# Optimization experiments

Hardware: AMD Instinct MI355X
Metric: run time of the kernel (lower is better)

Reference implementation:

```python
import jax, jax.numpy as jnp
import numpy as np

NUM_HEADS = 12


def setup_inputs() -> dict:
    key = jax.random.key(0)
    ks = jax.random.split(key, 6)
    B, N, C = 16, 576, 768
    H, D = NUM_HEADS, 768 // NUM_HEADS
    P = 16
    x = jax.random.normal(ks[0], (B, N, C), dtype=jnp.float32)
    prompt = jax.random.normal(ks[1], (B, 2, P, H, D), dtype=jnp.float32)
    act_scale = jax.random.uniform(ks[2], (2,), dtype=jnp.float32)
    qkv_w = jax.random.normal(ks[3], (3 * C, C), dtype=jnp.float32) * (C ** -0.5)
    proj_w = jax.random.normal(ks[4], (C, C), dtype=jnp.float32) * (C ** -0.5)
    proj_b = jnp.zeros((C,), dtype=jnp.float32)
    return {"x": x, "prompt": prompt, "act_scale": act_scale,
            "qkv_w": qkv_w, "proj_w": proj_w, "proj_b": proj_b}


def reference(x, prompt, act_scale, qkv_w, proj_w, proj_b):
    B, N, C = x.shape
    H = NUM_HEADS
    D = C // H
    scale = D ** -0.5
    # qkv projection: [B,N,3C] -> (3,B,H,N,D)
    qkv = (x @ qkv_w.T).reshape(B, N, 3, H, D).transpose(2, 0, 3, 1, 4)
    q, k, v = qkv[0], qkv[1], qkv[2]
    # prompt: [B,2,P,H,D] -> (2,B,H,P,D)
    pr = jnp.transpose(prompt, (1, 0, 3, 2, 4))
    key_prefix, value_prefix = pr[0], pr[1]        # [B,H,P,D]
    v = jnp.concatenate([value_prefix, v], axis=2)  # [B,H,P+N,D]
    # gated prefix scores
    prompt_attn = jnp.einsum('bhnd,bhpd->bhnp', q, key_prefix) * scale
    prompt_attn = prompt_attn + jnp.tanh(prompt_attn * act_scale[0]) * act_scale[1]
    # standard scores
    attn = jnp.einsum('bhnd,bhmd->bhnm', q, k) * scale
    attn = jnp.concatenate([prompt_attn, attn], axis=-1)  # [B,H,N,P+N]
    attn = jax.nn.softmax(attn, axis=-1)
    out = jnp.einsum('bhnm,bhmd->bhnd', attn, v)  # [B,H,N,D]
    out = out.transpose(0, 2, 1, 3).reshape(B, N, C)
    return out @ proj_w.T + proj_b
```

## Files before the change

### kernel.cpp

```cpp
#include <hip/hip_runtime.h>
#include <hip/hip_bf16.h>
#include <math.h>

namespace {

constexpr int kB = 16, kN = 576, kC = 768, kH = 12, kP = 16;
constexpr int kM = kB * kN;

typedef __attribute__((ext_vector_type(8))) __bf16 bf16x8;
typedef __attribute__((ext_vector_type(4))) float  f32x4;
typedef __attribute__((ext_vector_type(8))) unsigned short u16x8;

__device__ inline unsigned short f2bf(float f) {
  __bf16 h = (__bf16)f;
  return __builtin_bit_cast(unsigned short, h);
}
__device__ inline float bf2f(unsigned short u) {
  unsigned int x = ((unsigned int)u) << 16;
  return __builtin_bit_cast(float, x);
}
__device__ inline unsigned int pk2bf(float lo, float hi) {
  return (unsigned int)f2bf(lo) | ((unsigned int)f2bf(hi) << 16);
}
__device__ inline int xcd_swz(int hw, int nwg) {
  const int per = nwg >> 3;
  return (hw & 7) * per + (hw >> 3);
}

__global__ __launch_bounds__(256)
void cvt3(const float* __restrict__ x, const float* __restrict__ wq,
          const float* __restrict__ wp, unsigned short* __restrict__ xo,
          unsigned short* __restrict__ wqo, unsigned short* __restrict__ wpo) {
  const int bid = blockIdx.x;
  const float* in; unsigned short* out; int base;
  if (bid < 6912)       { in = x;  out = xo;  base = bid; }
  else if (bid < 8640)  { in = wq; out = wqo; base = bid - 6912; }
  else                  { in = wp; out = wpo; base = bid - 8640; }
  const int i = base * 256 + threadIdx.x;
  const float4 v = ((const float4*)in)[i];
  ((ushort4*)out)[i] = make_ushort4(f2bf(v.x), f2bf(v.y), f2bf(v.z), f2bf(v.w));
}

template<int OB>
__global__ __launch_bounds__(256)
void gemm_bf16(const unsigned short* __restrict__ A, const unsigned short* __restrict__ W,
               const float* __restrict__ bias, void* __restrict__ Yv, int Kd, int Nd) {
  __shared__ __align__(16) unsigned short As[2][4096];
  __shared__ __align__(16) unsigned short Bs[2][4096];
  const int tid  = threadIdx.x;
  const int wv   = tid >> 6, lane = tid & 63;
  const int gx   = Nd >> 7;
  const int lg   = xcd_swz(blockIdx.x, gridDim.x);
  const long bm  = (long)(lg / gx) * 128;
  const long bn  = (long)(lg % gx) * 128;
  const int wr   = (wv >> 1) * 64;
  const int wc   = (wv & 1) * 64;
  const int row15 = lane & 15, kg = lane >> 4;

  auto stage = [&](int buf, int kt) {
#pragma unroll
    for (int site = 0; site < 2; ++site) {
      const int p = site * 256 + tid;
      const unsigned short* srcA = A + (bm + (p >> 2)) * (long)Kd + kt + (p & 3) * 8;
      const unsigned short* srcB = W + (bn + (p >> 2)) * (long)Kd + kt + (p & 3) * 8;
      __builtin_amdgcn_global_load_lds(
          (const __attribute__((address_space(1))) unsigned int*)srcA,
          (__attribute__((address_space(3))) unsigned int*)(&As[buf][site * 2048 + wv * 512]),
          16, 0, 0);
      __builtin_amdgcn_global_load_lds(
          (const __attribute__((address_space(1))) unsigned int*)srcB,
          (__attribute__((address_space(3))) unsigned int*)(&Bs[buf][site * 2048 + wv * 512]),
          16, 0, 0);
    }
  };

  f32x4 acc[4][4] = {};
  stage(0, 0);
  __syncthreads();

  const int nt = Kd >> 5;
  for (int t = 0; t < nt; ++t) {
    const int cur = t & 1;
    if (t + 1 < nt) stage(cur ^ 1, (t + 1) << 5);

    bf16x8 af[4], bf_[4];
#pragma unroll
    for (int mi = 0; mi < 4; ++mi)
      af[mi] = *(const bf16x8*)(&As[cur][(wr + mi * 16 + row15) * 32 + kg * 8]);
#pragma unroll
    for (int ni = 0; ni < 4; ++ni)
      bf_[ni] = *(const bf16x8*)(&Bs[cur][(wc + ni * 16 + row15) * 32 + kg * 8]);
#pragma unroll
    for (int mi = 0; mi < 4; ++mi)
#pragma unroll
      for (int ni = 0; ni < 4; ++ni)
        acc[mi][ni] = __builtin_amdgcn_mfma_f32_16x16x32_bf16(af[mi], bf_[ni], acc[mi][ni], 0, 0, 0);
    __syncthreads();
  }

  const int r4 = kg * 4;
#pragma unroll
  for (int ni = 0; ni < 4; ++ni) {
    const long col = bn + wc + ni * 16 + row15;
    if constexpr (OB) {
      unsigned short* Y = (unsigned short*)Yv;
#pragma unroll
      for (int mi = 0; mi < 4; ++mi)
#pragma unroll
        for (int j = 0; j < 4; ++j)
          Y[(bm + wr + mi * 16 + r4 + j) * (long)Nd + col] = f2bf(acc[mi][ni][j]);
    } else {
      float* Y = (float*)Yv;
      const float bv = bias ? bias[col] : 0.0f;
#pragma unroll
      for (int mi = 0; mi < 4; ++mi)
#pragma unroll
        for (int j = 0; j < 4; ++j)
          Y[(bm + wr + mi * 16 + r4 + j) * (long)Nd + col] = acc[mi][ni][j] + bv;
    }
  }
}

__global__ __launch_bounds__(384, 4)
void attn_mfma(const unsigned short* __restrict__ qkv, const float* __restrict__ prompt,
               const float* __restrict__ act_scale, unsigned short* __restrict__ attn_out) {
  const int lg = xcd_swz(blockIdx.x, gridDim.x);
  const int qt = lg % 6, bh = lg / 6;
  const int h = bh % kH, b = bh / kH;
  const int tid = threadIdx.x, wv = tid >> 6, lane = tid & 63;
  const int q15 = lane & 15, kg = lane >> 4;

  __shared__ __align__(16) unsigned short Klds[2][4096];
  __shared__ __align__(16) unsigned short Vt[2][4096];
  __shared__ __align__(16) unsigned short Plds[6][1024];

  const float a0 = act_scale[0], a1 = act_scale[1];
  const int sw  = q15 & 7;
  const int sl0 = (kg ^ sw) << 3;
  const int sl1 = ((4 + kg) ^ sw) << 3;

  bf16x8 qf[2];
  {
    const unsigned short* qrow = qkv + (size_t)(b * kN + qt * 96 + wv * 16 + q15) * 2304 + h * 64;
#pragma unroll
    for (int dh = 0; dh < 2; ++dh) {
      u16x8 raw = *(const u16x8*)(qrow + dh * 32 + kg * 8);
      u16x8 sc;
#pragma unroll
      for (int j = 0; j < 8; ++j) sc[j] = f2bf(bf2f(raw[j]) * 0.125f);
      qf[dh] = __builtin_bit_cast(bf16x8, sc);
    }
  }

  if (tid < 128) {
    const int r = tid >> 3, s = tid & 7;
    const float* src = prompt + (((size_t)(b * 2) * kP + r) * kH + h) * 64 + s * 8;
    const float4 f0 = *(const float4*)src, f1 = *(const float4*)(src + 4);
    *(uint4*)(&Klds[0][r * 64 + ((s ^ (r & 7)) << 3)]) =
        make_uint4(pk2bf(f0.x, f0.y), pk2bf(f0.z, f0.w), pk2bf(f1.x, f1.y), pk2bf(f1.z, f1.w));
  }
  if (tid < 256) {
    const int vkp = tid & 15, vdg = tid >> 4;
    unsigned int w[4] = {0, 0, 0, 0};
    if (vkp < 8) {
      const float* s0 = prompt + (((size_t)(b * 2 + 1) * kP + 2 * vkp) * kH + h) * 64 + vdg * 4;
      const float* s1 = s0 + kH * 64;
      const float4 x0 = *(const float4*)s0;
      const float4 y0 = *(const float4*)s1;
      w[0] = pk2bf(x0.x, y0.x); w[1] = pk2bf(x0.y, y0.y);
      w[2] = pk2bf(x0.z, y0.z); w[3] = pk2bf(x0.w, y0.w);
    }
#pragma unroll
    for (int j = 0; j < 4; ++j) {
      const int d = vdg * 4 + j;
      Plds[0][0] += 0;
      *(unsigned int*)(&Vt[0][d * 64 + (((vkp >> 2) ^ (d & 7)) << 3) + (vkp & 3) * 2]) = w[j];
    }
  }
  __syncthreads();

  f32x4 o[4] = {};
  float mrun = -3.0e38f, lrun = 0.0f;

  const int vkp = tid & 31;
  const int vdg = (tid >> 5) & 7;

  for (int ch = 0; ch < 10; ++ch) {
    const int cur = ch & 1;

    u16x8 vld0, vld1;
    const bool doV = (ch < 9) && (wv < 4);
    if (ch < 9) {
      if (doV) {
        const int nv = ch * 64 + 2 * vkp;
        const unsigned short* s0 = qkv + (size_t)(b * kN + nv) * 2304 + 1536 + h * 64 + vdg * 8;
        vld0 = *(const u16x8*)s0;
        vld1 = *(const u16x8*)(s0 + 2304);
      } else if (wv >= 4) {
        const int rbase = (wv - 4) * 32;
#pragma unroll
        for (int g = 0; g < 4; ++g) {
          const int r = rbase + g * 8 + (lane >> 3), s = lane & 7;
          const unsigned short* src =
              qkv + (size_t)(b * kN + ch * 64 + r) * 2304 + 768 + h * 64 + ((s ^ (r & 7)) << 3);
          __builtin_amdgcn_global_load_lds(
              (const __attribute__((address_space(1))) unsigned int*)src,
              (__attribute__((address_space(3))) unsigned int*)(&Klds[cur ^ 1][(rbase + g * 8) * 64]),
              16, 0, 0);
        }
      }
    }

    f32x4 c[4];
    const int nkb = (ch == 0) ? 1 : 4;
#pragma unroll
    for (int kb = 0; kb < 4; ++kb) {
      if (kb < nkb) {
        const unsigned short* krow = &Klds[cur][(kb * 16 + q15) * 64];
        const bf16x8 k0 = *(const bf16x8*)(krow + sl0);
        const bf16x8 k1 = *(const bf16x8*)(krow + sl1);
        f32x4 t = {};
        t = __builtin_amdgcn_mfma_f32_16x16x32_bf16(k0, qf[0], t, 0, 0, 0);
        c[kb] = __builtin_amdgcn_mfma_f32_16x16x32_bf16(k1, qf[1], t, 0, 0, 0);
      } else {
        c[kb][0] = c[kb][1] = c[kb][2] = c[kb][3] = -1.0e30f;
      }
    }
    if (ch == 0) {
#pragma unroll
      for (int j = 0; j < 4; ++j) {
        const float s = c[0][j];
        const float e = __expf(2.0f * s * a0);
        c[0][j] = s + ((e - 1.0f) / (e + 1.0f)) * a1;
      }
    }

    float cmax = -3.0e38f;
#pragma unroll
    for (int kb = 0; kb < 4; ++kb)
#pragma unroll
      for (int j = 0; j < 4; ++j) cmax = fmaxf(cmax, c[kb][j]);
    cmax = fmaxf(cmax, __shfl_xor(cmax, 16, 64));
    cmax = fmaxf(cmax, __shfl_xor(cmax, 32, 64));
    if (!__all(cmax - mrun <= 8.0f)) {
      const float mnew = fmaxf(mrun, cmax);
      const float resc = __expf(mrun - mnew);
      lrun *= resc;
      float rq[4];
#pragma unroll
      for (int jr = 0; jr < 4; ++jr) rq[jr] = __shfl(resc, kg * 4 + jr, 64);
#pragma unroll
      for (int nb = 0; nb < 4; ++nb)
#pragma unroll
        for (int jr = 0; jr < 4; ++jr) o[nb][jr] *= rq[jr];
      mrun = mnew;
    }
    float pe[16];
    float psum = 0.0f;
#pragma unroll
    for (int kb = 0; kb < 4; ++kb)
#pragma unroll
      for (int j = 0; j < 4; ++j) { pe[kb * 4 + j] = __expf(c[kb][j] - mrun); psum += pe[kb * 4 + j]; }
    psum += __shfl_xor(psum, 16, 64);
    psum += __shfl_xor(psum, 32, 64);
    lrun += psum;

    {
      unsigned short* pl = &Plds[wv][q15 * 64];
#pragma unroll
      for (int kb = 0; kb < 4; ++kb) {
        const int off = (((kb * 2 + (kg >> 1)) ^ sw) << 3) + (kg & 1) * 4;
        *(uint2*)(pl + off) = make_uint2(pk2bf(pe[kb * 4], pe[kb * 4 + 1]),
                                         pk2bf(pe[kb * 4 + 2], pe[kb * 4 + 3]));
      }
    }
    if (doV) {
#pragma unroll
      for (int j = 0; j < 8; ++j) {
        const int d = vdg * 8 + j;
        *(unsigned int*)(&Vt[cur ^ 1][d * 64 + (((vkp >> 2) ^ (d & 7)) << 3) + (vkp & 3) * 2]) =
            (unsigned int)vld0[j] | ((unsigned int)vld1[j] << 16);
      }
    }

    const unsigned short* pw = &Plds[wv][q15 * 64];
    const bf16x8 pa0 = *(const bf16x8*)(pw + sl0);
    const bf16x8 pa1 = *(const bf16x8*)(pw + sl1);
#pragma unroll
    for (int nb = 0; nb < 4; ++nb) {
      const unsigned short* vr = &Vt[cur][(nb * 16 + q15) * 64];
      const bf16x8 bv0 = *(const bf16x8*)(vr + sl0);
      o[nb] = __builtin_amdgcn_mfma_f32_16x16x32_bf16(pa0, bv0, o[nb], 0, 0, 0);
      if (ch != 0) {
        const bf16x8 bv1 = *(const bf16x8*)(vr + sl1);
        o[nb] = __builtin_amdgcn_mfma_f32_16x16x32_bf16(pa1, bv1, o[nb], 0, 0, 0);
      }
    }

    __syncthreads();
  }

  const float inv = 1.0f / lrun;
  float iq[4];
#pragma unroll
  for (int jr = 0; jr < 4; ++jr) iq[jr] = __shfl(inv, kg * 4 + jr, 64);
  unsigned short* obase = attn_out + (size_t)(b * kN + qt * 96 + wv * 16) * 768 + h * 64;
#pragma unroll
  for (int nb = 0; nb < 4; ++nb)
#pragma unroll
    for (int jr = 0; jr < 4; ++jr)
      obase[(size_t)(kg * 4 + jr) * 768 + nb * 16 + q15] = f2bf(o[nb][jr] * iq[jr]);
}

}

extern "C" void kernel_launch(void* const* d_in, const int* in_sizes, int n_in,
                              void* d_out, int out_size, void* d_ws, size_t ws_size,
                              hipStream_t stream) {
  const float* x         = (const float*)d_in[0];
  const float* prompt    = (const float*)d_in[1];
  const float* act_scale = (const float*)d_in[2];
  const float* qkv_w     = (const float*)d_in[3];
  const float* proj_w    = (const float*)d_in[4];
  const float* proj_b    = (const float*)d_in[5];
  float* out = (float*)d_out;

  char* ws = (char*)d_ws;
  unsigned short* qkvb   = (unsigned short*)ws;
  unsigned short* xa     = (unsigned short*)(ws + 42467328);
  unsigned short* qkvwb  = (unsigned short*)(ws + 42467328 + 14155776);
  unsigned short* projwb = (unsigned short*)(ws + 42467328 + 14155776 + 3538944);

  cvt3<<<9216, 256, 0, stream>>>(x, qkv_w, proj_w, xa, qkvwb, projwb);

  gemm_bf16<1><<<(3 * kC / 128) * (kM / 128), 256, 0, stream>>>(xa, qkvwb, nullptr, qkvb, kC, 3 * kC);
  attn_mfma<<<(kN / 96) * kH * kB, 384, 0, stream>>>(qkvb, prompt, act_scale, xa);
  gemm_bf16<0><<<(kC / 128) * (kM / 128), 256, 0, stream>>>(xa, projwb, proj_b, out, kC, kC);
}
```

Measured before the change: 136.4 us.

## Process two query tiles per wave in attention to reuse K/V fragments

The attention kernel drops from 6 waves of 16 query rows to 3 waves of 32 rows each, so every K and V fragment read from LDS feeds two MFMAs. V staging moves to 2 waves and K async loads to 1 wave. The prefix V padding is explicitly zeroed so the first chunk can run the full PV MFMA without a branch. s_setprio is added around the MFMA sections. The change trades fewer waves per block, and possibly lower occupancy, for more register reuse and fewer LDS reads.

After: 129.5 us. 5.1% less time.

```diff
diff --git a/kernel.cpp b/kernel.cpp
--- a/kernel.cpp
+++ b/kernel.cpp
@@ -26,6 +26,10 @@
   const int per = nwg >> 3;
   return (hw & 7) * per + (hw >> 3);
 }
+
+#define GLDS16(src, dst) __builtin_amdgcn_global_load_lds( \
+    (const __attribute__((address_space(1))) unsigned int*)(src), \
+    (__attribute__((address_space(3))) unsigned int*)(dst), 16, 0, 0)
 
 __global__ __launch_bounds__(256)
 void cvt3(const float* __restrict__ x, const float* __restrict__ wq,
@@ -63,14 +67,8 @@
       const int p = site * 256 + tid;
       const unsigned short* srcA = A + (bm + (p >> 2)) * (long)Kd + kt + (p & 3) * 8;
       const unsigned short* srcB = W + (bn + (p >> 2)) * (long)Kd + kt + (p & 3) * 8;
-      __builtin_amdgcn_global_load_lds(
-          (const __attribute__((address_space(1))) unsigned int*)srcA,
-          (__attribute__((address_space(3))) unsigned int*)(&As[buf][site * 2048 + wv * 512]),
-          16, 0, 0);
-      __builtin_amdgcn_global_load_lds(
-          (const __attribute__((address_space(1))) unsigned int*)srcB,
-          (__attribute__((address_space(3))) unsigned int*)(&Bs[buf][site * 2048 + wv * 512]),
-          16, 0, 0);
+      GLDS16(srcA, &As[buf][site * 2048 + wv * 512]);
+      GLDS16(srcB, &Bs[buf][site * 2048 + wv * 512]);
     }
   };
 
@@ -121,7 +119,46 @@
   }
 }
 
-__global__ __launch_bounds__(384, 4)
+__device__ inline void softmax_group(f32x4 (&c)[4], float& mrun, float& lrun,
+                                     f32x4 (&o)[4], unsigned short* pl,
+                                     const int kg, const int sw) {
+  float cmax = -3.0e38f;
+#pragma unroll
+  for (int kb = 0; kb < 4; ++kb)
+#pragma unroll
+    for (int j = 0; j < 4; ++j) cmax = fmaxf(cmax, c[kb][j]);
+  cmax = fmaxf(cmax, __shfl_xor(cmax, 16, 64));
+  cmax = fmaxf(cmax, __shfl_xor(cmax, 32, 64));
+  if (!__all(cmax - mrun <= 8.0f)) {
+    const float mnew = fmaxf(mrun, cmax);
+    const float resc = __expf(mrun - mnew);
+    lrun *= resc;
+    float rq[4];
+#pragma unroll
+    for (int jr = 0; jr < 4; ++jr) rq[jr] = __shfl(resc, kg * 4 + jr, 64);
+#pragma unroll
+    for (int nb = 0; nb < 4; ++nb)
+#pragma unroll
+      for (int jr = 0; jr < 4; ++jr) o[nb][jr] *= rq[jr];
+    mrun = mnew;
+  }
+  float psum = 0.0f;
+#pragma unroll
+  for (int kb = 0; kb < 4; ++kb) {
+    const float p0 = __expf(c[kb][0] - mrun);
+    const float p1 = __expf(c[kb][1] - mrun);
+    const float p2 = __expf(c[kb][2] - mrun);
+    const float p3 = __expf(c[kb][3] - mrun);
+    psum += (p0 + p1) + (p2 + p3);
+    const int off = (((kb * 2 + (kg >> 1)) ^ sw) << 3) + (kg & 1) * 4;
+    *(uint2*)(pl + off) = make_uint2(pk2bf(p0, p1), pk2bf(p2, p3));
+  }
+  psum += __shfl_xor(psum, 16, 64);
+  psum += __shfl_xor(psum, 32, 64);
+  lrun += psum;
+}
+
+__global__ __launch_bounds__(192, 3)
 void attn_mfma(const unsigned short* __restrict__ qkv, const float* __restrict__ prompt,
                const float* __restrict__ act_scale, unsigned short* __restrict__ attn_out) {
   const int lg = xcd_swz(blockIdx.x, gridDim.x);
@@ -132,184 +169,169 @@
 
   __shared__ __align__(16) unsigned short Klds[2][4096];
   __shared__ __align__(16) unsigned short Vt[2][4096];
-  __shared__ __align__(16) unsigned short Plds[6][1024];
+  __shared__ __align__(16) unsigned short Plds[3][2048];
 
   const float a0 = act_scale[0], a1 = act_scale[1];
   const int sw  = q15 & 7;
   const int sl0 = (kg ^ sw) << 3;
   const int sl1 = ((4 + kg) ^ sw) << 3;
 
-  bf16x8 qf[2];
-  {
-    const unsigned short* qrow = qkv + (size_t)(b * kN + qt * 96 + wv * 16 + q15) * 2304 + h * 64;
+  bf16x8 qf[2][2];
+#pragma unroll
+  for (int g = 0; g < 2; ++g) {
+    const unsigned short* qrow =
+        qkv + (size_t)(b * kN + qt * 96 + wv * 32 + g * 16 + q15) * 2304 + h * 64;
 #pragma unroll
     for (int dh = 0; dh < 2; ++dh) {
       u16x8 raw = *(const u16x8*)(qrow + dh * 32 + kg * 8);
       u16x8 sc;
 #pragma unroll
       for (int j = 0; j < 8; ++j) sc[j] = f2bf(bf2f(raw[j]) * 0.125f);
-      qf[dh] = __builtin_bit_cast(bf16x8, sc);
+      qf[g][dh] = __builtin_bit_cast(bf16x8, sc);
     }
   }
 
   if (tid < 128) {
     const int r = tid >> 3, s = tid & 7;
     const float* src = prompt + (((size_t)(b * 2) * kP + r) * kH + h) * 64 + s * 8;
-    const float4 f0 = *(const float4*)src, f1 = *(const float4*)(src + 4);
+    const f32x4 f0 = *(const f32x4*)src, f1 = *(const f32x4*)(src + 4);
     *(uint4*)(&Klds[0][r * 64 + ((s ^ (r & 7)) << 3)]) =
-        make_uint4(pk2bf(f0.x, f0.y), pk2bf(f0.z, f0.w), pk2bf(f1.x, f1.y), pk2bf(f1.z, f1.w));
-  }
-  if (tid < 256) {
-    const int vkp = tid & 15, vdg = tid >> 4;
-    unsigned int w[4] = {0, 0, 0, 0};
-    if (vkp < 8) {
-      const float* s0 = prompt + (((size_t)(b * 2 + 1) * kP + 2 * vkp) * kH + h) * 64 + vdg * 4;
-      const float* s1 = s0 + kH * 64;
-      const float4 x0 = *(const float4*)s0;
-      const float4 y0 = *(const float4*)s1;
-      w[0] = pk2bf(x0.x, y0.x); w[1] = pk2bf(x0.y, y0.y);
-      w[2] = pk2bf(x0.z, y0.z); w[3] = pk2bf(x0.w, y0.w);
-    }
+        make_uint4(pk2bf(f0[0], f0[1]), pk2bf(f0[2], f0[3]),
+                   pk2bf(f1[0], f1[1]), pk2bf(f1[2], f1[3]));
+  }
+  if (tid < 128) {
+    const int kp = tid & 7, vdq = tid >> 3;
+    const float* s0 = prompt + (((size_t)(b * 2 + 1) * kP + 2 * kp) * kH + h) * 64 + vdq * 4;
+    const f32x4 x0 = *(const f32x4*)s0;
+    const f32x4 y0 = *(const f32x4*)(s0 + kH * 64);
 #pragma unroll
     for (int j = 0; j < 4; ++j) {
-      const int d = vdg * 4 + j;
-      Plds[0][0] += 0;
-      *(unsigned int*)(&Vt[0][d * 64 + (((vkp >> 2) ^ (d & 7)) << 3) + (vkp & 3) * 2]) = w[j];
-    }
+      const int d = vdq * 4 + j;
+      *(unsigned int*)(&Vt[0][d * 64 + (((kp >> 2) ^ (d & 7)) << 3) + (kp & 3) * 2]) =
+          pk2bf(x0[j], y0[j]);
+    }
+  }
+#pragma unroll
+  for (int i = 0; i < 2; ++i) {
+    const int idx = tid + 192 * i;
+    const int d = idx / 6, szl = (idx % 6) + 2;
+    *(uint4*)(&Vt[0][d * 64 + ((szl ^ (d & 7)) << 3)]) = make_uint4(0, 0, 0, 0);
   }
   __syncthreads();
 
-  f32x4 o[4] = {};
-  float mrun = -3.0e38f, lrun = 0.0f;
-
-  const int vkp = tid & 31;
-  const int vdg = (tid >> 5) & 7;
+  f32x4 o0[4] = {}, o1[4] = {};
+  float m0 = -3.0e38f, l0 = 0.0f, m1 = -3.0e38f, l1 = 0.0f;
+
+  const int vkp  = tid & 31;
+  const int vdgb = tid >> 5;
+  const int kr8  = lane >> 3, ks8 = lane & 7;
 
   for (int ch = 0; ch < 10; ++ch) {
     const int cur = ch & 1;
 
-    u16x8 vld0, vld1;
-    const bool doV = (ch < 9) && (wv < 4);
+    u16x8 va0, va1, vb0, vb1;
+    const bool doV = (ch < 9) && (wv < 2);
     if (ch < 9) {
       if (doV) {
-        const int nv = ch * 64 + 2 * vkp;
-        const unsigned short* s0 = qkv + (size_t)(b * kN + nv) * 2304 + 1536 + h * 64 + vdg * 8;
-        vld0 = *(const u16x8*)s0;
-        vld1 = *(const u16x8*)(s0 + 2304);
-      } else if (wv >= 4) {
-        const int rbase = (wv - 4) * 32;
-#pragma unroll
-        for (int g = 0; g < 4; ++g) {
-          const int r = rbase + g * 8 + (lane >> 3), s = lane & 7;
+        const unsigned short* r0 = qkv + (size_t)(b * kN + ch * 64 + 2 * vkp) * 2304 + 1536 + h * 64;
+        va0 = *(const u16x8*)(r0 + vdgb * 8);
+        va1 = *(const u16x8*)(r0 + (vdgb + 4) * 8);
+        vb0 = *(const u16x8*)(r0 + 2304 + vdgb * 8);
+        vb1 = *(const u16x8*)(r0 + 2304 + (vdgb + 4) * 8);
+      } else if (wv == 2) {
+#pragma unroll
+        for (int g8 = 0; g8 < 8; ++g8) {
+          const int r = g8 * 8 + kr8;
           const unsigned short* src =
-              qkv + (size_t)(b * kN + ch * 64 + r) * 2304 + 768 + h * 64 + ((s ^ (r & 7)) << 3);
-          __builtin_amdgcn_global_load_lds(
-              (const __attribute__((address_space(1))) unsigned int*)src,
-              (__attribute__((address_space(3))) unsigned int*)(&Klds[cur ^ 1][(rbase + g * 8) * 64]),
-              16, 0, 0);
+              qkv + (size_t)(b * kN + ch * 64 + r) * 2304 + 768 + h * 64 + ((ks8 ^ (r & 7)) << 3);
+          GLDS16(src, &Klds[cur ^ 1][g8 * 512]);
         }
       }
     }
 
-    f32x4 c[4];
-    const int nkb = (ch == 0) ? 1 : 4;
+    f32x4 c0[4], c1[4];
+    __builtin_amdgcn_s_setprio(1);
 #pragma unroll
     for (int kb = 0; kb < 4; ++kb) {
-      if (kb < nkb) {
+      if (ch == 0 && kb > 0) {
+        c0[kb][0] = c0[kb][1] = c0[kb][2] = c0[kb][3] = -1.0e30f;
+        c1[kb][0] = c1[kb][1] = c1[kb][2] = c1[kb][3] = -1.0e30f;
+      } else {
         const unsigned short* krow = &Klds[cur][(kb * 16 + q15) * 64];
         const bf16x8 k0 = *(const bf16x8*)(krow + sl0);
         const bf16x8 k1 = *(const bf16x8*)(krow + sl1);
-        f32x4 t = {};
-        t = __builtin_amdgcn_mfma_f32_16x16x32_bf16(k0, qf[0], t, 0, 0, 0);
-        c[kb] = __builtin_amdgcn_mfma_f32_16x16x32_bf16(k1, qf[1], t, 0, 0, 0);
-      } else {
-        c[kb][0] = c[kb][1] = c[kb][2] = c[kb][3] = -1.0e30f;
+        f32x4 t0 = {}, t1 = {};
+        t0 = __builtin_amdgcn_mfma_f32_16x16x32_bf16(k0, qf[0][0], t0, 0, 0, 0);
+        c0[kb] = __builtin_amdgcn_mfma_f32_16x16x32_bf16(k1, qf[0][1], t0, 0, 0, 0);
+        t1 = __builtin_amdgcn_mfma_f32_16x16x32_bf16(k0, qf[1][0], t1, 0, 0, 0);
+        c1[kb] = __builtin_amdgcn_mfma_f32_16x16x32_bf16(k1, qf[1][1], t1, 0, 0, 0);
       }
     }
+    __builtin_amdgcn_s_setprio(0);
     if (ch == 0) {
 #pragma unroll
       for (int j = 0; j < 4; ++j) {
-        const float s = c[0][j];
-        const float e = __expf(2.0f * s * a0);
-        c[0][j] = s + ((e - 1.0f) / (e + 1.0f)) * a1;
+        const float s0v = c0[0][j];
+        const float e0 = __expf(2.0f * s0v * a0);
+        c0[0][j] = s0v + ((e0 - 1.0f) / (e0 + 1.0f)) * a1;
+        const float s1v = c1[0][j];
+        const float e1 = __expf(2.0f * s1v * a0);
+        c1[0][j] = s1v + ((e1 - 1.0f) / (e1 + 1.0f)) * a1;
       }
     }
 
-    float cmax = -3.0e38f;
-#pragma unroll
-    for (int kb = 0; kb < 4; ++kb)
-#pragma unroll
-      for (int j = 0; j < 4; ++j) cmax = fmaxf(cmax, c[kb][j]);
-    cmax = fmaxf(cmax, __shfl_xor(cmax, 16, 64));
-    cmax = fmaxf(cmax, __shfl_xor(cmax, 32, 64));
-    if (!__all(cmax - mrun <= 8.0f)) {
-      const float mnew = fmaxf(mrun, cmax);
-      const float resc = __expf(mrun - mnew);
-      lrun *= resc;
-      float rq[4];
-#pragma unroll
-      for (int jr = 0; jr < 4; ++jr) rq[jr] = __shfl(resc, kg * 4 + jr, 64);
-#pragma unroll
-      for (int nb = 0; nb < 4; ++nb)
-#pragma unroll
-        for (int jr = 0; jr < 4; ++jr) o[nb][jr] *= rq[jr];
-      mrun = mnew;
-    }
-    float pe[16];
-    float psum = 0.0f;
-#pragma unroll
-    for (int kb = 0; kb < 4; ++kb)
-#pragma unroll
-      for (int j = 0; j < 4; ++j) { pe[kb * 4 + j] = __expf(c[kb][j] - mrun); psum += pe[kb * 4 + j]; }
-    psum += __shfl_xor(psum, 16, 64);
-    psum += __shfl_xor(psum, 32, 64);
-    lrun += psum;
-
-    {
-      unsigned short* pl = &Plds[wv][q15 * 64];
-#pragma unroll
-      for (int kb = 0; kb < 4; ++kb) {
-        const int off = (((kb * 2 + (kg >> 1)) ^ sw) << 3) + (kg & 1) * 4;
-        *(uint2*)(pl + off) = make_uint2(pk2bf(pe[kb * 4], pe[kb * 4 + 1]),
-                                         pk2bf(pe[kb * 4 + 2], pe[kb * 4 + 3]));
+    softmax_group(c0, m0, l0, o0, &Plds[wv][q15 * 64], kg, sw);
+    softmax_group(c1, m1, l1, o1, &Plds[wv][(q15 + 16) * 64], kg, sw);
+
+    if (doV) {
+#pragma unroll
+      for (int j = 0; j < 8; ++j) {
+        const int d0 = vdgb * 8 + j;
+        *(unsigned int*)(&Vt[cur ^ 1][d0 * 64 + (((vkp >> 2) ^ (d0 & 7)) << 3) + (vkp & 3) * 2]) =
+            (unsigned int)va0[j] | ((unsigned int)vb0[j] << 16);
+        const int d1 = (vdgb + 4) * 8 + j;
+        *(unsigned int*)(&Vt[cur ^ 1][d1 * 64 + (((vkp >> 2) ^ (d1 & 7)) << 3) + (vkp & 3) * 2]) =
+            (unsigned int)va1[j] | ((unsigned int)vb1[j] << 16);
       }
     }
-    if (doV) {
-#pragma unroll
-      for (int j = 0; j < 8; ++j) {
-        const int d = vdg * 8 + j;
-        *(unsigned int*)(&Vt[cur ^ 1][d * 64 + (((vkp >> 2) ^ (d & 7)) << 3) + (vkp & 3) * 2]) =
-            (unsigned int)vld0[j] | ((unsigned int)vld1[j] << 16);
-      }
-    }
-
-    const unsigned short* pw = &Plds[wv][q15 * 64];
-    const bf16x8 pa0 = *(const bf16x8*)(pw + sl0);
-    const bf16x8 pa1 = *(const bf16x8*)(pw + sl1);
+
+    const unsigned short* p0 = &Plds[wv][q15 * 64];
+    const unsigned short* p1 = &Plds[wv][(q15 + 16) * 64];
+    const bf16x8 pa00 = *(const bf16x8*)(p0 + sl0);
+    const bf16x8 pa01 = *(const bf16x8*)(p0 + sl1);
+    const bf16x8 pa10 = *(const bf16x8*)(p1 + sl0);
+    const bf16x8 pa11 = *(const bf16x8*)(p1 + sl1);
+    __builtin_amdgcn_s_setprio(1);
 #pragma unroll
     for (int nb = 0; nb < 4; ++nb) {
       const unsigned short* vr = &Vt[cur][(nb * 16 + q15) * 64];
       const bf16x8 bv0 = *(const bf16x8*)(vr + sl0);
-      o[nb] = __builtin_amdgcn_mfma_f32_16x16x32_bf16(pa0, bv0, o[nb], 0, 0, 0);
-      if (ch != 0) {
-        const bf16x8 bv1 = *(const bf16x8*)(vr + sl1);
-        o[nb] = __builtin_amdgcn_mfma_f32_16x16x32_bf16(pa1, bv1, o[nb], 0, 0, 0);
-      }
-    }
+      const bf16x8 bv1 = *(const bf16x8*)(vr + sl1);
+      o0[nb] = __builtin_amdgcn_mfma_f32_16x16x32_bf16(pa00, bv0, o0[nb], 0, 0, 0);
+      o0[nb] = __builtin_amdgcn_mfma_f32_16x16x32_bf16(pa01, bv1, o0[nb], 0, 0, 0);
+      o1[nb] = __builtin_amdgcn_mfma_f32_16x16x32_bf16(pa10, bv0, o1[nb], 0, 0, 0);
+      o1[nb] = __builtin_amdgcn_mfma_f32_16x16x32_bf16(pa11, bv1, o1[nb], 0, 0, 0);
+    }
+    __builtin_amdgcn_s_setprio(0);
 
     __syncthreads();
   }
 
-  const float inv = 1.0f / lrun;
-  float iq[4];
-#pragma unroll
-  for (int jr = 0; jr < 4; ++jr) iq[jr] = __shfl(inv, kg * 4 + jr, 64);
-  unsigned short* obase = attn_out + (size_t)(b * kN + qt * 96 + wv * 16) * 768 + h * 64;
+  const float i0 = 1.0f / l0, i1 = 1.0f / l1;
+  float iq0[4], iq1[4];
+#pragma unroll
+  for (int jr = 0; jr < 4; ++jr) {
+    iq0[jr] = __shfl(i0, kg * 4 + jr, 64);
+    iq1[jr] = __shfl(i1, kg * 4 + jr, 64);
+  }
+  unsigned short* ob = attn_out + (size_t)(b * kN + qt * 96 + wv * 32) * 768 + h * 64;
 #pragma unroll
   for (int nb = 0; nb < 4; ++nb)
 #pragma unroll
-    for (int jr = 0; jr < 4; ++jr)
-      obase[(size_t)(kg * 4 + jr) * 768 + nb * 16 + q15] = f2bf(o[nb][jr] * iq[jr]);
+    for (int jr = 0; jr < 4; ++jr) {
+      ob[(size_t)(kg * 4 + jr) * 768 + nb * 16 + q15] = f2bf(o0[nb][jr] * iq0[jr]);
+      ob[(size_t)(16 + kg * 4 + jr) * 768 + nb * 16 + q15] = f2bf(o1[nb][jr] * iq1[jr]);
+    }
 }
 
 }
@@ -334,6 +356,6 @@
   cvt3<<<9216, 256, 0, stream>>>(x, qkv_w, proj_w, xa, qkvwb, projwb);
 
   gemm_bf16<1><<<(3 * kC / 128) * (kM / 128), 256, 0, stream>>>(xa, qkvwb, nullptr, qkvb, kC, 3 * kC);
-  attn_mfma<<<(kN / 96) * kH * kB, 384, 0, stream>>>(qkvb, prompt, act_scale, xa);
+  attn_mfma<<<(kN / 96) * kH * kB, 192, 0, stream>>>(qkvb, prompt, act_scale, xa);
   gemm_bf16<0><<<(kC / 128) * (kM / 128), 256, 0, stream>>>(xa, projwb, proj_b, out, kC, kC);
 }
```
